# Kernel tuning notes

Hardware: AMD Instinct MI355X
Metric: run time of the kernel (lower is better)

The kernel has to match this reference:

```python
import jax, jax.numpy as jnp
import numpy as np

P_W, P_H = 4, 8            # patch_size=[4,8]: p[0]=width, p[1]=height
EMBED, DEPTH, HEADS = 384, 12, 6
HD = EMBED // HEADS        # 64
THETA = 100.0
LN_EPS = 1e-5


def axial_freqs(pw, ph):
    # compute_axial_cis(dim=HD, end_x=pw, end_y=ph): angles for x and y axes, as cos/sin
    f = 1.0 / THETA ** (np.arange(0, HD, 4)[: HD // 4].astype(np.float32) / HD)  # (16,)
    t = np.arange(pw * ph, dtype=np.float32)
    tx, ty = t % pw, np.floor(t / pw)
    ang = np.concatenate([np.outer(tx, f), np.outer(ty, f)], -1)  # (N, 32)
    return jnp.asarray(np.cos(ang)), jnp.asarray(np.sin(ang))


def patchify(img):
    # (3, h, w) -> (ph*pw, 3*P_H*P_W), matching view/permute in NaViT_ROPE.forward
    c, h, w = img.shape
    ph, pw = h // P_H, w // P_W
    seq = img.reshape(c, ph, P_H, pw, P_W).transpose(1, 3, 0, 2, 4).reshape(ph * pw, -1)
    return seq, ph, pw


def layer_norm(x, w, b):
    m = x.mean(-1, keepdims=True)
    v = ((x - m) ** 2).mean(-1, keepdims=True)
    return (x - m) / jnp.sqrt(v + LN_EPS) * w + b


def rope(x, cos, sin):
    # x: (B,H,N,HD) paired as (...,HD//2,2); cos/sin: (B,N,HD//2)
    xp = x.reshape(*x.shape[:-1], -1, 2)
    x0, x1 = xp[..., 0], xp[..., 1]
    c, s = cos[:, None], sin[:, None]
    return jnp.stack([x0 * c - x1 * s, x0 * s + x1 * c], -1).reshape(x.shape)


def forward(imgs, params):
    (pe_ln_in_w, pe_ln_in_b, pe_w, pe_ln_out_w, pe_ln_out_b, blk, lnf_w, lnf_b) = params
    seqs, coss, sins, lens = [], [], [], []
    for img in imgs:
        seq, ph, pw = patchify(img)
        c, s = axial_freqs(pw, ph)
        seqs.append(seq); coss.append(c); sins.append(s); lens.append(seq.shape[0])
    nmax = max(lens)
    pad = lambda a: jnp.pad(a, ((0, nmax - a.shape[0]), (0, 0)))
    x = jnp.stack([pad(s) for s in seqs])      # (B, Nmax, 96)
    cos = jnp.stack([pad(c) for c in coss])    # (B, Nmax, 32)
    sin = jnp.stack([pad(s) for s in sins])
    mask = jnp.arange(nmax)[None, :] >= jnp.array(lens)[:, None]        # (B, Nmax), True = pad
    attn_bias = jnp.where(mask, -jnp.inf, 0.0)[:, None, None, :]        # (B,1,1,Nmax)

    # patch embed: LN(96) -> Linear(96,384,no bias) -> LN(384)
    x = layer_norm(x, pe_ln_in_w, pe_ln_in_b) @ pe_w
    x = layer_norm(x, pe_ln_out_w, pe_ln_out_b)

    scale = HD ** -0.5

    def block(x, p):
        ln1_w, ln1_b, qkv_w, qkv_b, proj_w, proj_b, ln2_w, ln2_b, fc1_w, fc1_b, fc2_w, fc2_b = p
        B, N, C = x.shape
        h = layer_norm(x, ln1_w, ln1_b)
        qkv = (h @ qkv_w + qkv_b).reshape(B, N, 3, HEADS, HD).transpose(2, 0, 3, 1, 4)
        q, k, v = qkv[0], qkv[1], qkv[2]
        q, k = rope(q, cos, sin), rope(k, cos, sin)
        attn = jnp.einsum('bhnd,bhmd->bhnm', q * scale, k) + attn_bias
        attn = jax.nn.softmax(attn, axis=-1)
        o = jnp.einsum('bhnm,bhmd->bhnd', attn, v).transpose(0, 2, 1, 3).reshape(B, N, C)
        x = x + (o @ proj_w + proj_b)
        h2 = layer_norm(x, ln2_w, ln2_b)
        h2 = jax.nn.gelu(h2 @ fc1_w + fc1_b, approximate=False)  # torch nn.GELU default (erf)
        x = x + (h2 @ fc2_w + fc2_b)
        return x, None

    x, _ = jax.lax.scan(block, x, blk)
    x = layer_norm(x, lnf_w, lnf_b)
    return x, mask


def setup_inputs() -> dict:
    key = jax.random.key(0)
    ks = jax.random.split(key, 10)
    sizes = [(3, 32, 512), (3, 32, 768), (3, 32, 896), (3, 32, 1024)]
    pd = 3 * P_H * P_W  # 96
    w = lambda k, sh: jax.random.normal(k, sh, jnp.float32) * 0.02
    inp = {}
    for i, s in enumerate(sizes):
        inp[f'img{i}'] = jax.random.normal(ks[i], s, jnp.float32)
    inp.update(
        pe_ln_in_w=jnp.ones((pd,), jnp.float32), pe_ln_in_b=jnp.zeros((pd,), jnp.float32),
        pe_w=w(ks[4], (pd, EMBED)),
        pe_ln_out_w=jnp.ones((EMBED,), jnp.float32), pe_ln_out_b=jnp.zeros((EMBED,), jnp.float32),
        ln1_w=jnp.ones((DEPTH, EMBED), jnp.float32), ln1_b=jnp.zeros((DEPTH, EMBED), jnp.float32),
        qkv_w=w(ks[5], (DEPTH, EMBED, 3 * EMBED)), qkv_b=jnp.zeros((DEPTH, 3 * EMBED), jnp.float32),
        proj_w=w(ks[6], (DEPTH, EMBED, EMBED)), proj_b=jnp.zeros((DEPTH, EMBED), jnp.float32),
        ln2_w=jnp.ones((DEPTH, EMBED), jnp.float32), ln2_b=jnp.zeros((DEPTH, EMBED), jnp.float32),
        fc1_w=w(ks[7], (DEPTH, EMBED, 4 * EMBED)), fc1_b=jnp.zeros((DEPTH, 4 * EMBED), jnp.float32),
        fc2_w=w(ks[8], (DEPTH, 4 * EMBED, EMBED)), fc2_b=jnp.zeros((DEPTH, EMBED), jnp.float32),
        lnf_w=jnp.ones((EMBED,), jnp.float32), lnf_b=jnp.zeros((EMBED,), jnp.float32),
    )
    return inp


def reference(img0, img1, img2, img3, pe_ln_in_w, pe_ln_in_b, pe_w, pe_ln_out_w, pe_ln_out_b,
              ln1_w, ln1_b, qkv_w, qkv_b, proj_w, proj_b, ln2_w, ln2_b,
              fc1_w, fc1_b, fc2_w, fc2_b, lnf_w, lnf_b):
    blk = (ln1_w, ln1_b, qkv_w, qkv_b, proj_w, proj_b, ln2_w, ln2_b, fc1_w, fc1_b, fc2_w, fc2_b)
    return forward([img0, img1, img2, img3],
                   (pe_ln_in_w, pe_ln_in_b, pe_w, pe_ln_out_w, pe_ln_out_b, blk, lnf_w, lnf_b))
```

## Files before the change

kernel.cpp:

```cpp
#include <hip/hip_runtime.h>


#define EMBED 384
#define NHEADS 6
#define HD 64
#define NSEQ 1024
#define NB 4
#define NROWS (NB * NSEQ)
#define PD 96
#define NZ 2

typedef __attribute__((ext_vector_type(8))) short bf16x8;
typedef __attribute__((ext_vector_type(4))) float f32x4;

__constant__ int c_lens[4] = {512, 768, 896, 1024};

__device__ __forceinline__ unsigned f2bf(float f) {
    unsigned u = __float_as_uint(f);
    return (u + 0x7fffu + ((u >> 16) & 1u)) >> 16;
}
__device__ __forceinline__ float bf2f(unsigned short h) {
    return __uint_as_float(((unsigned)h) << 16);
}

__global__ void patchify_kernel(const float* __restrict__ i0, const float* __restrict__ i1,
                                const float* __restrict__ i2, const float* __restrict__ i3,
                                float* __restrict__ xin, float* __restrict__ cosT,
                                float* __restrict__ sinT) {
    int bn = blockIdx.x;
    int b = bn >> 10, n = bn & 1023;
    const int lens[4] = {512, 768, 896, 1024};
    const int pws[4]  = {128, 192, 224, 256};
    const float* imgs[4] = {i0, i1, i2, i3};
    int len = lens[b], pw = pws[b];
    int W = pw * 4;
    int t = threadIdx.x;
    float* xrow = xin + (size_t)bn * PD;
    if (n < len) {
        int pr = n / pw, pc = n - pr * pw;
        const float* img = imgs[b];
        if (t < PD) {
            int c = t >> 5, py = (t >> 2) & 7, px = t & 3;
            xrow[t] = img[(size_t)c * 32 * W + (size_t)(pr * 8 + py) * W + pc * 4 + px];
        }
        if (t < 32) {
            int j = t & 15;
            float fr = powf(100.0f, -(float)j / 16.0f);
            float coord = (t < 16) ? (float)pc : (float)pr;
            float ang = coord * fr;
            cosT[(size_t)bn * 32 + t] = cosf(ang);
            sinT[(size_t)bn * 32 + t] = sinf(ang);
        }
    } else {
        if (t < PD) xrow[t] = 0.f;
        if (t < 32) { cosT[(size_t)bn * 32 + t] = 0.f; sinT[(size_t)bn * 32 + t] = 0.f; }
    }
}

__global__ void convT_kernel(const float* __restrict__ src, unsigned short* __restrict__ dst,
                             int K, int N, int Kpad) {
    __shared__ float tile[32][33];
    int k0 = blockIdx.x * 32, n0 = blockIdx.y * 32, l = blockIdx.z;
    int t = threadIdx.x;
    {
        int kk = t >> 3, nn = (t & 7) * 4;
        float4 v = make_float4(0.f, 0.f, 0.f, 0.f);
        if (k0 + kk < K)
            v = *(const float4*)(src + ((size_t)l * K + (k0 + kk)) * N + n0 + nn);
        tile[kk][nn + 0] = v.x; tile[kk][nn + 1] = v.y;
        tile[kk][nn + 2] = v.z; tile[kk][nn + 3] = v.w;
    }
    __syncthreads();
    {
        int nn = t >> 3, kk = (t & 7) * 4;
        unsigned lo = f2bf(tile[kk + 0][nn]) | (f2bf(tile[kk + 1][nn]) << 16);
        unsigned hi = f2bf(tile[kk + 2][nn]) | (f2bf(tile[kk + 3][nn]) << 16);
        uint2 u = make_uint2(lo, hi);
        *(uint2*)(dst + (size_t)l * N * Kpad + (size_t)(n0 + nn) * Kpad + k0 + kk) = u;
    }
}

template <int C, int OS, bool OBF>
__global__ void ln_kernel(const float* __restrict__ in, const float* __restrict__ w,
                          const float* __restrict__ bias, void* __restrict__ outv) {
    int row = blockIdx.x * 4 + (threadIdx.x >> 6);
    int t = threadIdx.x & 63;
    const float* x = in + (size_t)row * C;
    constexpr int NE = (C + 63) / 64;
    float vals[NE];
    float s = 0.f;
#pragma unroll
    for (int i = 0; i < NE; i++) {
        int e = t + i * 64;
        float v = (e < C) ? x[e] : 0.f;
        vals[i] = v; s += v;
    }
#pragma unroll
    for (int off = 32; off; off >>= 1) s += __shfl_down(s, off);
    float mean = __shfl(s, 0) / (float)C;
    float vs = 0.f;
#pragma unroll
    for (int i = 0; i < NE; i++) {
        int e = t + i * 64;
        float d = (e < C) ? (vals[i] - mean) : 0.f;
        vs += d * d;
    }
#pragma unroll
    for (int off = 32; off; off >>= 1) vs += __shfl_down(vs, off);
    float rstd = rsqrtf(__shfl(vs, 0) / (float)C + 1e-5f);
    constexpr int NO = (OS + 63) / 64;
#pragma unroll
    for (int i = 0; i < NO; i++) {
        int e = t + i * 64;
        if (e < OS) {
            float v = (e < C) ? ((vals[i] - mean) * rstd * w[e] + bias[e]) : 0.f;
            if (OBF) ((unsigned short*)outv)[(size_t)row * OS + e] = (unsigned short)f2bf(v);
            else     ((float*)outv)[(size_t)row * OS + e] = v;
        }
    }
}

template <int FLAGS>
__global__ __launch_bounds__(256) void gemm_bf16(
    const unsigned short* __restrict__ A, const unsigned short* __restrict__ Wt,
    const float* __restrict__ bias, const float* __restrict__ res,
    float* __restrict__ outf, unsigned short* __restrict__ outb,
    int M, int K, int N) {
    __shared__ unsigned short As[64][72];
    __shared__ unsigned short Bs[64][72];
    int t = threadIdx.x;
    int wid = t >> 6, lane = t & 63;
    int m0 = blockIdx.y * 64, n0 = blockIdx.x * 64;
    int wm = (wid >> 1) * 32, wn = (wid & 1) * 32;
    f32x4 acc[2][2] = {};
    int srow = t >> 2, sc = (t & 3) * 8;
    const unsigned short* Ap = A + (size_t)(m0 + srow) * K + sc;
    const unsigned short* Bp = Wt + (size_t)(n0 + srow) * K + sc;
    int lr = lane & 15, lk = (lane >> 4) * 8;
    for (int k0 = 0; k0 < K; k0 += 64) {
        *(uint4*)&As[srow][sc]      = *(const uint4*)(Ap + k0);
        *(uint4*)&As[srow][sc + 32] = *(const uint4*)(Ap + k0 + 32);
        *(uint4*)&Bs[srow][sc]      = *(const uint4*)(Bp + k0);
        *(uint4*)&Bs[srow][sc + 32] = *(const uint4*)(Bp + k0 + 32);
        __syncthreads();
#pragma unroll
        for (int kk = 0; kk < 64; kk += 32) {
            bf16x8 a0 = *(const bf16x8*)&As[wm + lr][kk + lk];
            bf16x8 a1 = *(const bf16x8*)&As[wm + 16 + lr][kk + lk];
            bf16x8 b0 = *(const bf16x8*)&Bs[wn + lr][kk + lk];
            bf16x8 b1 = *(const bf16x8*)&Bs[wn + 16 + lr][kk + lk];
            acc[0][0] = __builtin_amdgcn_mfma_f32_16x16x32_bf16(a0, b0, acc[0][0], 0, 0, 0);
            acc[0][1] = __builtin_amdgcn_mfma_f32_16x16x32_bf16(a0, b1, acc[0][1], 0, 0, 0);
            acc[1][0] = __builtin_amdgcn_mfma_f32_16x16x32_bf16(a1, b0, acc[1][0], 0, 0, 0);
            acc[1][1] = __builtin_amdgcn_mfma_f32_16x16x32_bf16(a1, b1, acc[1][1], 0, 0, 0);
        }
        __syncthreads();
    }
    int lq = lane >> 4;
#pragma unroll
    for (int mi = 0; mi < 2; mi++)
#pragma unroll
        for (int ni = 0; ni < 2; ni++) {
#pragma unroll
            for (int r = 0; r < 4; r++) {
                int grow = m0 + wm + mi * 16 + lq * 4 + r;
                int gcol = n0 + wn + ni * 16 + lr;
                float v = acc[mi][ni][r];
                if (FLAGS & 1) v += bias[gcol];
                if (FLAGS & 2) v = 0.5f * v * (1.f + erff(v * 0.70710678118654752f));
                if (FLAGS & 4) v += res[(size_t)grow * N + gcol];
                if (FLAGS & 8) outb[(size_t)grow * N + gcol] = (unsigned short)f2bf(v);
                else           outf[(size_t)grow * N + gcol] = v;
            }
        }
}

template <int FLAGS>
__global__ __launch_bounds__(256) void gemm_bf16_128(
    const unsigned short* __restrict__ A, const unsigned short* __restrict__ Wt,
    const float* __restrict__ bias, const float* __restrict__ res,
    float* __restrict__ outf, unsigned short* __restrict__ outb,
    int M, int K, int N) {
    __shared__ unsigned short As[128][72];
    __shared__ unsigned short Bs[128][72];
    int t = threadIdx.x;
    int wid = t >> 6, lane = t & 63;
    int m0 = blockIdx.y * 128, n0 = blockIdx.x * 128;
    int wm = (wid >> 1) * 64, wn = (wid & 1) * 64;
    f32x4 acc[4][4] = {};
    int srow = t >> 3, sc = (t & 7) * 8;
    const unsigned short* Ap = A + (size_t)(m0 + srow) * K + sc;
    const unsigned short* Bp = Wt + (size_t)(n0 + srow) * K + sc;
    int lr = lane & 15, lk = (lane >> 4) * 8;
    for (int k0 = 0; k0 < K; k0 += 64) {
#pragma unroll
        for (int rr = 0; rr < 4; rr++) {
            *(uint4*)&As[srow + rr * 32][sc] = *(const uint4*)(Ap + (size_t)(rr * 32) * K + k0);
            *(uint4*)&Bs[srow + rr * 32][sc] = *(const uint4*)(Bp + (size_t)(rr * 32) * K + k0);
        }
        __syncthreads();
#pragma unroll
        for (int kk = 0; kk < 64; kk += 32) {
            bf16x8 af[4], bfr[4];
#pragma unroll
            for (int i = 0; i < 4; i++) af[i]  = *(const bf16x8*)&As[wm + i * 16 + lr][kk + lk];
#pragma unroll
            for (int j = 0; j < 4; j++) bfr[j] = *(const bf16x8*)&Bs[wn + j * 16 + lr][kk + lk];
#pragma unroll
            for (int i = 0; i < 4; i++)
#pragma unroll
                for (int j = 0; j < 4; j++)
                    acc[i][j] = __builtin_amdgcn_mfma_f32_16x16x32_bf16(af[i], bfr[j], acc[i][j], 0, 0, 0);
        }
        __syncthreads();
    }
    int lq = lane >> 4;
#pragma unroll
    for (int mi = 0; mi < 4; mi++)
#pragma unroll
        for (int ni = 0; ni < 4; ni++) {
#pragma unroll
            for (int r = 0; r < 4; r++) {
                int grow = m0 + wm + mi * 16 + lq * 4 + r;
                int gcol = n0 + wn + ni * 16 + lr;
                float v = acc[mi][ni][r];
                if (FLAGS & 1) v += bias[gcol];
                if (FLAGS & 2) v = 0.5f * v * (1.f + erff(v * 0.70710678118654752f));
                if (FLAGS & 4) v += res[(size_t)grow * N + gcol];
                if (FLAGS & 8) outb[(size_t)grow * N + gcol] = (unsigned short)f2bf(v);
                else           outf[(size_t)grow * N + gcol] = v;
            }
        }
}

__global__ __launch_bounds__(256) void gemm_qkv_rope(
    const unsigned short* __restrict__ A, const unsigned short* __restrict__ Wt,
    const float* __restrict__ bias, const float* __restrict__ cosT,
    const float* __restrict__ sinT, unsigned short* __restrict__ qr,
    unsigned short* __restrict__ kr, unsigned short* __restrict__ vt) {
    const int K = 384;
    __shared__ unsigned short As[64][72];
    __shared__ unsigned short Bs[64][72];
    int t = threadIdx.x;
    int wid = t >> 6, lane = t & 63;
    int m0 = blockIdx.y * 64, n0 = blockIdx.x * 64;
    int wm = (wid >> 1) * 32, wn = (wid & 1) * 32;
    f32x4 acc[2][2] = {};
    int srow = t >> 2, sc = (t & 3) * 8;
    const unsigned short* Ap = A + (size_t)(m0 + srow) * K + sc;
    const unsigned short* Bp = Wt + (size_t)(n0 + srow) * K + sc;
    int lr = lane & 15, lk = (lane >> 4) * 8;
    for (int k0 = 0; k0 < K; k0 += 64) {
        *(uint4*)&As[srow][sc]      = *(const uint4*)(Ap + k0);
        *(uint4*)&As[srow][sc + 32] = *(const uint4*)(Ap + k0 + 32);
        *(uint4*)&Bs[srow][sc]      = *(const uint4*)(Bp + k0);
        *(uint4*)&Bs[srow][sc + 32] = *(const uint4*)(Bp + k0 + 32);
        __syncthreads();
#pragma unroll
        for (int kk = 0; kk < 64; kk += 32) {
            bf16x8 a0 = *(const bf16x8*)&As[wm + lr][kk + lk];
            bf16x8 a1 = *(const bf16x8*)&As[wm + 16 + lr][kk + lk];
            bf16x8 b0 = *(const bf16x8*)&Bs[wn + lr][kk + lk];
            bf16x8 b1 = *(const bf16x8*)&Bs[wn + 16 + lr][kk + lk];
            acc[0][0] = __builtin_amdgcn_mfma_f32_16x16x32_bf16(a0, b0, acc[0][0], 0, 0, 0);
            acc[0][1] = __builtin_amdgcn_mfma_f32_16x16x32_bf16(a0, b1, acc[0][1], 0, 0, 0);
            acc[1][0] = __builtin_amdgcn_mfma_f32_16x16x32_bf16(a1, b0, acc[1][0], 0, 0, 0);
            acc[1][1] = __builtin_amdgcn_mfma_f32_16x16x32_bf16(a1, b1, acc[1][1], 0, 0, 0);
        }
        __syncthreads();
    }
    int lq = lane >> 4;
    int bx = blockIdx.x;
    int sec = bx / 6, hh = bx - sec * 6;
    if (sec == 2) {
#pragma unroll
        for (int mi = 0; mi < 2; mi++)
#pragma unroll
            for (int ni = 0; ni < 2; ni++) {
                int d = wn + ni * 16 + lr;
                float bb = bias[768 + hh * 64 + d];
                int g0 = m0 + wm + mi * 16 + lq * 4;
                int b = g0 >> 10, n = g0 & 1023;
                uint2 u;
                u.x = f2bf(acc[mi][ni][0] + bb) | (f2bf(acc[mi][ni][1] + bb) << 16);
                u.y = f2bf(acc[mi][ni][2] + bb) | (f2bf(acc[mi][ni][3] + bb) << 16);
                *(uint2*)&vt[((size_t)(b * 6 + hh) * HD + d) * NSEQ + n] = u;
            }
    } else {
        unsigned short* dst = sec ? kr : qr;
        float scl = sec ? 1.0f : 0.125f;
#pragma unroll
        for (int mi = 0; mi < 2; mi++)
#pragma unroll
            for (int ni = 0; ni < 2; ni++) {
                int d = wn + ni * 16 + lr;
                float bb = bias[sec * 384 + hh * 64 + d];
                int pp = d >> 1;
#pragma unroll
                for (int r = 0; r < 4; r++) {
                    int grow = m0 + wm + mi * 16 + lq * 4 + r;
                    float v = acc[mi][ni][r] + bb;
                    float c = cosT[(size_t)grow * 32 + pp];
                    float s = sinT[(size_t)grow * 32 + pp];
                    float vp = __shfl_xor(v, 1);
                    float out = ((d & 1) == 0 ? v * c - vp * s : vp * s + v * c) * scl;
                    int b = grow >> 10, n = grow & 1023;
                    dst[((size_t)(b * 6 + hh) * NSEQ + n) * HD + d] = (unsigned short)f2bf(out);
                }
            }
    }
}

__global__ __launch_bounds__(256) void attn_mfma(
    const unsigned short* __restrict__ qr, const unsigned short* __restrict__ kr,
    const unsigned short* __restrict__ vt, unsigned short* __restrict__ opart,
    float* __restrict__ mP, float* __restrict__ lP) {
    __shared__ unsigned short Ks[64][72];
    __shared__ unsigned short Vs[64][72];
    __shared__ unsigned short Pb[4][16][72];
    __shared__ float Aw[4][16];
    int bh = blockIdx.x;
    int q0 = blockIdx.y * 64;
    int z  = blockIdx.z;
    int len = c_lens[bh / 6];
    int T = len >> 6;
    int t0 = (T * z) >> 1, t1 = (T * (z + 1)) >> 1;
    int t = threadIdx.x, wid = t >> 6, lane = t & 63;
    int lz = lane & 15, lq = lane >> 4;
    const unsigned short* Qp = qr + ((size_t)bh * NSEQ + q0 + wid * 16 + lz) * HD + lq * 8;
    bf16x8 qa0 = *(const bf16x8*)(Qp);
    bf16x8 qa1 = *(const bf16x8*)(Qp + 32);
    int srow = t >> 2, sc = (t & 3) * 16;
    const unsigned short* Kp = kr + (size_t)bh * NSEQ * HD + (size_t)srow * HD + sc;
    const unsigned short* Vp = vt + ((size_t)bh * HD + srow) * NSEQ + sc;
    f32x4 oacc[4] = {};
    float m_s = -1e30f, l_s = 0.f;
    for (int kt = t0; kt < t1; kt++) {
        int k0 = kt << 6;
        __syncthreads();
        *(uint4*)&Ks[srow][sc]     = *(const uint4*)(Kp + (size_t)k0 * HD);
        *(uint4*)&Ks[srow][sc + 8] = *(const uint4*)(Kp + (size_t)k0 * HD + 8);
        *(uint4*)&Vs[srow][sc]     = *(const uint4*)(Vp + k0);
        *(uint4*)&Vs[srow][sc + 8] = *(const uint4*)(Vp + k0 + 8);
        __syncthreads();
        f32x4 s[4] = {};
#pragma unroll
        for (int g = 0; g < 4; g++) {
            bf16x8 kf0 = *(const bf16x8*)&Ks[g * 16 + lz][lq * 8];
            bf16x8 kf1 = *(const bf16x8*)&Ks[g * 16 + lz][32 + lq * 8];
            s[g] = __builtin_amdgcn_mfma_f32_16x16x32_bf16(kf0, qa0, s[g], 0, 0, 0);
            s[g] = __builtin_amdgcn_mfma_f32_16x16x32_bf16(kf1, qa1, s[g], 0, 0, 0);
        }
        float mx = s[0][0];
#pragma unroll
        for (int g = 0; g < 4; g++)
#pragma unroll
            for (int r = 0; r < 4; r++) mx = fmaxf(mx, s[g][r]);
        mx = fmaxf(mx, __shfl_xor(mx, 16));
        mx = fmaxf(mx, __shfl_xor(mx, 32));
        float mn = fmaxf(m_s, mx);
        float a_s = __expf(m_s - mn);
        m_s = mn;
        float sum = 0.f;
#pragma unroll
        for (int g = 0; g < 4; g++)
#pragma unroll
            for (int r = 0; r < 4; r++) {
                float p = __expf(s[g][r] - mn);
                s[g][r] = p;
                sum += p;
            }
        sum += __shfl_xor(sum, 16);
        sum += __shfl_xor(sum, 32);
        l_s = l_s * a_s + sum;
        if (lq == 0) Aw[wid][lz] = a_s;
#pragma unroll
        for (int g = 0; g < 4; g++) {
            uint2 u;
            u.x = f2bf(s[g][0]) | (f2bf(s[g][1]) << 16);
            u.y = f2bf(s[g][2]) | (f2bf(s[g][3]) << 16);
            *(uint2*)&Pb[wid][lz][g * 16 + lq * 4] = u;
        }
        f32x4 al4 = *(const f32x4*)&Aw[wid][lq * 4];
        bf16x8 pa0 = *(const bf16x8*)&Pb[wid][lz][lq * 8];
        bf16x8 pa1 = *(const bf16x8*)&Pb[wid][lz][32 + lq * 8];
#pragma unroll
        for (int g = 0; g < 4; g++) {
#pragma unroll
            for (int r = 0; r < 4; r++) oacc[g][r] *= al4[r];
            bf16x8 vf0 = *(const bf16x8*)&Vs[g * 16 + lz][lq * 8];
            bf16x8 vf1 = *(const bf16x8*)&Vs[g * 16 + lz][32 + lq * 8];
            oacc[g] = __builtin_amdgcn_mfma_f32_16x16x32_bf16(pa0, vf0, oacc[g], 0, 0, 0);
            oacc[g] = __builtin_amdgcn_mfma_f32_16x16x32_bf16(pa1, vf1, oacc[g], 0, 0, 0);
        }
    }
    size_t rb = ((size_t)z * 24 + bh) * NSEQ + q0 + wid * 16;
    if (lq == 0) { mP[rb + lz] = m_s; lP[rb + lz] = l_s; }
#pragma unroll
    for (int r = 0; r < 4; r++) {
        int row = lq * 4 + r;
#pragma unroll
        for (int g = 0; g < 4; g++)
            opart[(rb + row) * HD + g * 16 + lz] = (unsigned short)f2bf(oacc[g][r]);
    }
}

__global__ __launch_bounds__(256) void gemm_proj_combine(
    const unsigned short* __restrict__ opart, const float* __restrict__ mP,
    const float* __restrict__ lP, const unsigned short* __restrict__ Wt,
    const float* __restrict__ bias, float* __restrict__ xio) {
    const int K = 384, N = 384;
    __shared__ unsigned short As[64][72];
    __shared__ unsigned short Bs[64][72];
    __shared__ float Winv[64][6][NZ];
    int t = threadIdx.x;
    int wid = t >> 6, lane = t & 63;
    int m0 = blockIdx.y * 64, n0 = blockIdx.x * 64;
    int wm = (wid >> 1) * 32, wn = (wid & 1) * 32;
    const size_t zstride = (size_t)24 * NSEQ * HD;
    for (int p = t; p < 384; p += 256) {
        int tok = p / 6, hh = p - tok * 6;
        int g = m0 + tok, b = g >> 10, n = g & 1023;
        int bh = b * 6 + hh;
        size_t i0 = (size_t)bh * NSEQ + n;
        float ma = mP[i0], mb = mP[i0 + (size_t)24 * NSEQ];
        float la = lP[i0], lb = lP[i0 + (size_t)24 * NSEQ];
        float ms = fmaxf(ma, mb);
        float wa = __expf(ma - ms), wb = __expf(mb - ms);
        float inv = 1.f / (la * wa + lb * wb);
        Winv[tok][hh][0] = wa * inv;
        Winv[tok][hh][1] = wb * inv;
    }
    __syncthreads();
    f32x4 acc[2][2] = {};
    int srow = t >> 2, sc = (t & 3) * 8;
    int gg = m0 + srow, gb = gg >> 10, gn = gg & 1023;
    const unsigned short* Bp = Wt + (size_t)(n0 + srow) * K + sc;
    int lr = lane & 15, lk = (lane >> 4) * 8;
    for (int k0 = 0; k0 < K; k0 += 64) {
#pragma unroll
        for (int h = 0; h < 2; h++) {
            int col = k0 + sc + h * 32;
            int hh = col >> 6, d = col & 63;
            int bh = gb * 6 + hh;
            size_t base = ((size_t)bh * NSEQ + gn) * HD + d;
            float w0 = Winv[srow][hh][0], w1 = Winv[srow][hh][1];
            uint4 u0 = *(const uint4*)&opart[base];
            uint4 u1 = *(const uint4*)&opart[base + zstride];
            unsigned a[4] = {u0.x, u0.y, u0.z, u0.w};
            unsigned c[4] = {u1.x, u1.y, u1.z, u1.w};
            uint4 outw;
            unsigned rr[4];
#pragma unroll
            for (int q = 0; q < 4; q++) {
                float lo = bf2f((unsigned short)(a[q] & 0xffff)) * w0 +
                           bf2f((unsigned short)(c[q] & 0xffff)) * w1;
                float hi = bf2f((unsigned short)(a[q] >> 16)) * w0 +
                           bf2f((unsigned short)(c[q] >> 16)) * w1;
                rr[q] = f2bf(lo) | (f2bf(hi) << 16);
            }
            outw.x = rr[0]; outw.y = rr[1]; outw.z = rr[2]; outw.w = rr[3];
            *(uint4*)&As[srow][sc + h * 32] = outw;
        }
        *(uint4*)&Bs[srow][sc]      = *(const uint4*)(Bp + k0);
        *(uint4*)&Bs[srow][sc + 32] = *(const uint4*)(Bp + k0 + 32);
        __syncthreads();
#pragma unroll
        for (int kk = 0; kk < 64; kk += 32) {
            bf16x8 a0 = *(const bf16x8*)&As[wm + lr][kk + lk];
            bf16x8 a1 = *(const bf16x8*)&As[wm + 16 + lr][kk + lk];
            bf16x8 b0 = *(const bf16x8*)&Bs[wn + lr][kk + lk];
            bf16x8 b1 = *(const bf16x8*)&Bs[wn + 16 + lr][kk + lk];
            acc[0][0] = __builtin_amdgcn_mfma_f32_16x16x32_bf16(a0, b0, acc[0][0], 0, 0, 0);
            acc[0][1] = __builtin_amdgcn_mfma_f32_16x16x32_bf16(a0, b1, acc[0][1], 0, 0, 0);
            acc[1][0] = __builtin_amdgcn_mfma_f32_16x16x32_bf16(a1, b0, acc[1][0], 0, 0, 0);
            acc[1][1] = __builtin_amdgcn_mfma_f32_16x16x32_bf16(a1, b1, acc[1][1], 0, 0, 0);
        }
        __syncthreads();
    }
    int lq = lane >> 4;
#pragma unroll
    for (int mi = 0; mi < 2; mi++)
#pragma unroll
        for (int ni = 0; ni < 2; ni++) {
#pragma unroll
            for (int r = 0; r < 4; r++) {
                int grow = m0 + wm + mi * 16 + lq * 4 + r;
                int gcol = n0 + wn + ni * 16 + lr;
                float v = acc[mi][ni][r] + bias[gcol] + xio[(size_t)grow * N + gcol];
                xio[(size_t)grow * N + gcol] = v;
            }
        }
}

__global__ void mask_kernel(float* __restrict__ mout) {
    int idx = blockIdx.x * 256 + threadIdx.x;
    if (idx >= NROWS) return;
    int b = idx >> 10, n = idx & 1023;
    mout[idx] = (n >= c_lens[b]) ? 1.0f : 0.0f;
}

extern "C" void kernel_launch(void* const* d_in, const int* in_sizes, int n_in,
                              void* d_out, int out_size, void* d_ws, size_t ws_size,
                              hipStream_t stream) {
    (void)in_sizes; (void)n_in; (void)out_size; (void)ws_size;
    const float* img0 = (const float*)d_in[0];
    const float* img1 = (const float*)d_in[1];
    const float* img2 = (const float*)d_in[2];
    const float* img3 = (const float*)d_in[3];
    const float* pe_ln_in_w  = (const float*)d_in[4];
    const float* pe_ln_in_b  = (const float*)d_in[5];
    const float* pe_w        = (const float*)d_in[6];
    const float* pe_ln_out_w = (const float*)d_in[7];
    const float* pe_ln_out_b = (const float*)d_in[8];
    const float* ln1_w  = (const float*)d_in[9];
    const float* ln1_b  = (const float*)d_in[10];
    const float* qkv_w  = (const float*)d_in[11];
    const float* qkv_b  = (const float*)d_in[12];
    const float* proj_w = (const float*)d_in[13];
    const float* proj_b = (const float*)d_in[14];
    const float* ln2_w  = (const float*)d_in[15];
    const float* ln2_b  = (const float*)d_in[16];
    const float* fc1_w  = (const float*)d_in[17];
    const float* fc1_b  = (const float*)d_in[18];
    const float* fc2_w  = (const float*)d_in[19];
    const float* fc2_b  = (const float*)d_in[20];
    const float* lnf_w  = (const float*)d_in[21];
    const float* lnf_b  = (const float*)d_in[22];

    char* ws = (char*)d_ws;
    float*          x_f    = (float*)(ws + 0);
    char*           R      = ws + 6291456;
    unsigned short* opart  = (unsigned short*)R;
    unsigned short* mlp_bf = (unsigned short*)R;
    unsigned short* h_bf   = (unsigned short*)(ws + 18874368);
    unsigned short* qr     = (unsigned short*)(ws + 22020096);
    unsigned short* kr     = (unsigned short*)(ws + 25165824);
    unsigned short* vt     = (unsigned short*)(ws + 28311552);
    float*          cosT   = (float*)(ws + 31457280);
    float*          sinT   = (float*)(ws + 31981568);
    float*          xin    = (float*)(ws + 32505856);
    float*          mPt    = xin;
    float*          lPt    = (float*)(ws + 32505856 + 393216);
    unsigned short* xln_bf = (unsigned short*)(ws + 34078720);
    unsigned short* pe_wt  = (unsigned short*)(ws + 35127296);
    unsigned short* qkv_wt = (unsigned short*)(ws + 35225600);
    unsigned short* proj_wt= (unsigned short*)(ws + 45842432);
    unsigned short* fc1_wt = (unsigned short*)(ws + 49381376);
    unsigned short* fc2_wt = (unsigned short*)(ws + 63537152);

    convT_kernel<<<dim3(4, 12, 1),   256, 0, stream>>>(pe_w,   pe_wt,   96,  EMBED, 128);
    convT_kernel<<<dim3(12, 36, 12), 256, 0, stream>>>(qkv_w,  qkv_wt,  384, 1152,  384);
    convT_kernel<<<dim3(12, 12, 12), 256, 0, stream>>>(proj_w, proj_wt, 384, 384,   384);
    convT_kernel<<<dim3(12, 48, 12), 256, 0, stream>>>(fc1_w,  fc1_wt,  384, 1536,  384);
    convT_kernel<<<dim3(48, 12, 12), 256, 0, stream>>>(fc2_w,  fc2_wt,  1536, 384,  1536);

    patchify_kernel<<<NROWS, 128, 0, stream>>>(img0, img1, img2, img3, xin, cosT, sinT);
    ln_kernel<PD, 128, true><<<NROWS / 4, 256, 0, stream>>>(xin, pe_ln_in_w, pe_ln_in_b, xln_bf);
    gemm_bf16<0><<<dim3(EMBED / 64, NROWS / 64), 256, 0, stream>>>(
        xln_bf, pe_wt, nullptr, nullptr, x_f, nullptr, NROWS, 128, EMBED);
    ln_kernel<EMBED, EMBED, false><<<NROWS / 4, 256, 0, stream>>>(x_f, pe_ln_out_w, pe_ln_out_b, x_f);

    for (int l = 0; l < 12; ++l) {
        ln_kernel<EMBED, EMBED, true><<<NROWS / 4, 256, 0, stream>>>(
            x_f, ln1_w + l * EMBED, ln1_b + l * EMBED, h_bf);
        gemm_qkv_rope<<<dim3(18, NROWS / 64), 256, 0, stream>>>(
            h_bf, qkv_wt + (size_t)l * 1152 * 384, qkv_b + (size_t)l * 1152,
            cosT, sinT, qr, kr, vt);
        attn_mfma<<<dim3(NB * NHEADS, NSEQ / 64, NZ), 256, 0, stream>>>(
            qr, kr, vt, opart, mPt, lPt);
        gemm_proj_combine<<<dim3(EMBED / 64, NROWS / 64), 256, 0, stream>>>(
            opart, mPt, lPt, proj_wt + (size_t)l * 384 * 384,
            proj_b + (size_t)l * EMBED, x_f);
        ln_kernel<EMBED, EMBED, true><<<NROWS / 4, 256, 0, stream>>>(
            x_f, ln2_w + l * EMBED, ln2_b + l * EMBED, h_bf);
        gemm_bf16_128<11><<<dim3(1536 / 128, NROWS / 128), 256, 0, stream>>>(
            h_bf, fc1_wt + (size_t)l * 1536 * 384, fc1_b + (size_t)l * 1536, nullptr,
            nullptr, mlp_bf, NROWS, EMBED, 1536);
        gemm_bf16<5><<<dim3(EMBED / 64, NROWS / 64), 256, 0, stream>>>(
            mlp_bf, fc2_wt + (size_t)l * 1536 * 384, fc2_b + (size_t)l * EMBED, x_f,
            x_f, nullptr, NROWS, 1536, EMBED);
    }

    ln_kernel<EMBED, EMBED, false><<<NROWS / 4, 256, 0, stream>>>(x_f, lnf_w, lnf_b, (float*)d_out);
    mask_kernel<<<16, 256, 0, stream>>>((float*)d_out + (size_t)NROWS * EMBED);
}
```

Measured before the change: 1.167 ms.

## Register-prefetch next K/V tile in attention and fold mask into final LN

The attention kernel now loads the next K/V tile from global memory into registers while the current tile's MFMAs run. This restructures the sync pattern to one barrier after the LDS store and one at loop end. MFMA sections are wrapped in s_setprio to favour matrix issue. Separately, the padding-mask output is written by the final layer-norm kernel, which removes a launch; the cost is extra register pressure in attention.

```diff
diff --git a/kernel.cpp b/kernel.cpp
--- a/kernel.cpp
+++ b/kernel.cpp
@@ -80,7 +80,7 @@
     }
 }
 
-template <int C, int OS, bool OBF>
+template <int C, int OS, bool OBF, bool MASK = false>
 __global__ void ln_kernel(const float* __restrict__ in, const float* __restrict__ w,
                           const float* __restrict__ bias, void* __restrict__ outv) {
     int row = blockIdx.x * 4 + (threadIdx.x >> 6);
@@ -117,6 +117,10 @@
             if (OBF) ((unsigned short*)outv)[(size_t)row * OS + e] = (unsigned short)f2bf(v);
             else     ((float*)outv)[(size_t)row * OS + e] = v;
         }
+    }
+    if (MASK && t == 0) {
+        int b = row >> 10, n = row & 1023;
+        ((float*)outv)[(size_t)NROWS * EMBED + row] = (n >= c_lens[b]) ? 1.0f : 0.0f;
     }
 }
 
@@ -335,15 +339,30 @@
     const unsigned short* Vp = vt + ((size_t)bh * HD + srow) * NSEQ + sc;
     f32x4 oacc[4] = {};
     float m_s = -1e30f, l_s = 0.f;
+    uint4 rk0, rk1, rv0, rv1;
+    {
+        int k0 = t0 << 6;
+        rk0 = *(const uint4*)(Kp + (size_t)k0 * HD);
+        rk1 = *(const uint4*)(Kp + (size_t)k0 * HD + 8);
+        rv0 = *(const uint4*)(Vp + k0);
+        rv1 = *(const uint4*)(Vp + k0 + 8);
+    }
     for (int kt = t0; kt < t1; kt++) {
-        int k0 = kt << 6;
-        __syncthreads();
-        *(uint4*)&Ks[srow][sc]     = *(const uint4*)(Kp + (size_t)k0 * HD);
-        *(uint4*)&Ks[srow][sc + 8] = *(const uint4*)(Kp + (size_t)k0 * HD + 8);
-        *(uint4*)&Vs[srow][sc]     = *(const uint4*)(Vp + k0);
-        *(uint4*)&Vs[srow][sc + 8] = *(const uint4*)(Vp + k0 + 8);
-        __syncthreads();
+        *(uint4*)&Ks[srow][sc]     = rk0;
+        *(uint4*)&Ks[srow][sc + 8] = rk1;
+        *(uint4*)&Vs[srow][sc]     = rv0;
+        *(uint4*)&Vs[srow][sc + 8] = rv1;
+        __syncthreads();
+        uint4 nk0, nk1, nv0, nv1;
+        if (kt + 1 < t1) {
+            int k1 = (kt + 1) << 6;
+            nk0 = *(const uint4*)(Kp + (size_t)k1 * HD);
+            nk1 = *(const uint4*)(Kp + (size_t)k1 * HD + 8);
+            nv0 = *(const uint4*)(Vp + k1);
+            nv1 = *(const uint4*)(Vp + k1 + 8);
+        }
         f32x4 s[4] = {};
+        __builtin_amdgcn_s_setprio(1);
 #pragma unroll
         for (int g = 0; g < 4; g++) {
             bf16x8 kf0 = *(const bf16x8*)&Ks[g * 16 + lz][lq * 8];
@@ -351,6 +370,7 @@
             s[g] = __builtin_amdgcn_mfma_f32_16x16x32_bf16(kf0, qa0, s[g], 0, 0, 0);
             s[g] = __builtin_amdgcn_mfma_f32_16x16x32_bf16(kf1, qa1, s[g], 0, 0, 0);
         }
+        __builtin_amdgcn_s_setprio(0);
         float mx = s[0][0];
 #pragma unroll
         for (int g = 0; g < 4; g++)
@@ -384,6 +404,7 @@
         f32x4 al4 = *(const f32x4*)&Aw[wid][lq * 4];
         bf16x8 pa0 = *(const bf16x8*)&Pb[wid][lz][lq * 8];
         bf16x8 pa1 = *(const bf16x8*)&Pb[wid][lz][32 + lq * 8];
+        __builtin_amdgcn_s_setprio(1);
 #pragma unroll
         for (int g = 0; g < 4; g++) {
 #pragma unroll
@@ -393,6 +414,9 @@
             oacc[g] = __builtin_amdgcn_mfma_f32_16x16x32_bf16(pa0, vf0, oacc[g], 0, 0, 0);
             oacc[g] = __builtin_amdgcn_mfma_f32_16x16x32_bf16(pa1, vf1, oacc[g], 0, 0, 0);
         }
+        __builtin_amdgcn_s_setprio(0);
+        __syncthreads();
+        rk0 = nk0; rk1 = nk1; rv0 = nv0; rv1 = nv1;
     }
     size_t rb = ((size_t)z * 24 + bh) * NSEQ + q0 + wid * 16;
     if (lq == 0) { mP[rb + lz] = m_s; lP[rb + lz] = l_s; }
@@ -491,13 +515,6 @@
                 xio[(size_t)grow * N + gcol] = v;
             }
         }
-}
-
-__global__ void mask_kernel(float* __restrict__ mout) {
-    int idx = blockIdx.x * 256 + threadIdx.x;
-    if (idx >= NROWS) return;
-    int b = idx >> 10, n = idx & 1023;
-    mout[idx] = (n >= c_lens[b]) ? 1.0f : 0.0f;
 }
 
 extern "C" void kernel_launch(void* const* d_in, const int* in_sizes, int n_in,
@@ -582,6 +599,6 @@
             x_f, nullptr, NROWS, 1536, EMBED);
     }
 
-    ln_kernel<EMBED, EMBED, false><<<NROWS / 4, 256, 0, stream>>>(x_f, lnf_w, lnf_b, (float*)d_out);
-    mask_kernel<<<16, 256, 0, stream>>>((float*)d_out + (size_t)NROWS * EMBED);
-}
+    ln_kernel<EMBED, EMBED, false, true><<<NROWS / 4, 256, 0, stream>>>(
+        x_f, lnf_w, lnf_b, (float*)d_out);
+}
```

Measured after the change: 1.149 ms. About the same (-1.5%).
